# Optimization experiments

Hardware: AMD Instinct MI355X
Metric: run time of the kernel (lower is better)

## Reference

```python
import jax, jax.numpy as jnp
import numpy as np
import math

B, N, D = 4, 16384, 256
M, H = 64, 8
HD = D // H

def setup_inputs() -> dict:
    key = jax.random.key(0)
    ks = jax.random.split(key, 5)
    s = 1.0 / math.sqrt(D)
    return {
        "x": jax.random.normal(ks[0], (B, N, D), dtype=jnp.float32),
        "Ws": jax.random.normal(ks[1], (M, D), dtype=jnp.float32) * s,
        "bs": jnp.zeros((M,), dtype=jnp.float32),
        "Wqkv": jax.random.normal(ks[2], (3 * D, D), dtype=jnp.float32) * s,
        "Wo": jax.random.normal(ks[3], (D, D), dtype=jnp.float32) * s,
        "bo": jnp.zeros((D,), dtype=jnp.float32),
    }

def reference(x, Ws, bs, Wqkv, Wo, bo):
    # slice weights: softmax over N (dim=1), matching the torch code exactly
    logits = jnp.einsum('bnd,md->bnm', x, Ws) + bs          # [B,N,M]
    weights = jax.nn.softmax(logits, axis=1)                # softmax over N
    # pooling: tokens[b,m,d] = sum_n w[b,n,m] * x[b,n,d]
    tokens = jnp.einsum('bnm,bnd->bmd', weights, x)         # [B,M,D]
    # qkv projection (no bias)
    qkv = jnp.einsum('bmd,ed->bme', tokens, Wqkv)           # [B,M,3D]
    qkv = qkv.reshape(B, M, 3, H, HD)
    q = qkv[:, :, 0].transpose(0, 2, 1, 3)                  # [B,H,M,HD]
    k = qkv[:, :, 1].transpose(0, 2, 1, 3)
    v = qkv[:, :, 2].transpose(0, 2, 1, 3)
    scale = 1.0 / math.sqrt(HD)
    attn = jax.nn.softmax(jnp.einsum('bhmd,bhkd->bhmk', q, k) * scale, axis=-1)
    token_out = jnp.einsum('bhmk,bhkd->bhmd', attn, v)      # [B,H,M,HD]
    token_out = token_out.transpose(0, 2, 1, 3).reshape(B, M, D)
    token_out = jnp.einsum('bmd,ed->bme', token_out, Wo) + bo
    # unpooling: out[b,n,d] = sum_m w[b,n,m] * token_out[b,m,d]
    out = jnp.einsum('bnm,bmd->bnd', weights, token_out)    # [B,N,D]
    return out
```

## Files before the change

kernel.cpp:

```cpp
#include <hip/hip_runtime.h>
#include <math.h>

constexpr int B = 4;
constexpr int N = 16384;
constexpr int D = 256;
constexpr int M = 64;
constexpr int H = 8;

typedef __attribute__((ext_vector_type(8))) short short8;
typedef __attribute__((ext_vector_type(4))) float floatx4;

__device__ __forceinline__ float4 ld4(const float* p) {
  return *reinterpret_cast<const float4*>(p);
}
__device__ __forceinline__ unsigned short f2bf(float f) {
  unsigned u = __float_as_uint(f);
  unsigned r = (u + 0x7fffu + ((u >> 16) & 1u)) >> 16;
  return (unsigned short)r;
}

__global__ __launch_bounds__(256) void k0_prep(
    const float* __restrict__ Ws, const float* __restrict__ Wqkv,
    const float* __restrict__ Wo, unsigned short* __restrict__ WsB,
    unsigned short* __restrict__ WqkvB, unsigned short* __restrict__ WoB,
    float* __restrict__ denom, float* __restrict__ tokens) {
  const int g = blockIdx.x * 256 + threadIdx.x;
  if (g < 32768)
    *reinterpret_cast<float2*>(&tokens[g * 2]) = make_float2(0.f, 0.f);
  if (g < 128)
    *reinterpret_cast<float2*>(&denom[g * 2]) = make_float2(0.f, 0.f);
  const float* src;
  unsigned short* dst;
  int off;
  if (g < 2048) {
    src = Ws; dst = WsB; off = g;
  } else if (g < 26624) {
    src = Wqkv; dst = WqkvB; off = g - 2048;
  } else {
    src = Wo; dst = WoB; off = g - 26624;
  }
  const float4 a = ld4(&src[(size_t)off * 8]);
  const float4 c = ld4(&src[(size_t)off * 8 + 4]);
  unsigned d0 = (unsigned)f2bf(a.x) | ((unsigned)f2bf(a.y) << 16);
  unsigned d1 = (unsigned)f2bf(a.z) | ((unsigned)f2bf(a.w) << 16);
  unsigned d2 = (unsigned)f2bf(c.x) | ((unsigned)f2bf(c.y) << 16);
  unsigned d3 = (unsigned)f2bf(c.z) | ((unsigned)f2bf(c.w) << 16);
  *reinterpret_cast<uint4*>(&dst[(size_t)off * 8]) = make_uint4(d0, d1, d2, d3);
}

__global__ __launch_bounds__(512, 4) void k1_fused(
    const float* __restrict__ x, const unsigned short* __restrict__ WsB,
    const float* __restrict__ bs, unsigned short* __restrict__ En,
    float* __restrict__ denom) {
  __shared__ unsigned short Wt[64][264];
  __shared__ float red[64];
  const int b = blockIdx.y;
  const int n0 = blockIdx.x * 128;
  const int tid = threadIdx.x;
  const int w = tid >> 6, l = tid & 63;
  const int l15 = l & 15;
  const int q8 = (l >> 4) * 8;
  const int ar = w * 16 + l15;

  float4 fx[16];
  const float* xrow = &x[((size_t)(b * N + n0 + ar)) * D];
#pragma unroll
  for (int ks = 0; ks < 8; ++ks) {
    fx[2 * ks] = ld4(&xrow[ks * 32 + q8]);
    fx[2 * ks + 1] = ld4(&xrow[ks * 32 + q8 + 4]);
  }
#pragma unroll
  for (int p = 0; p < 4; ++p) {
    const int u = p * 512 + tid;
    const int row = u >> 5;
    const int c = (u & 31) * 8;
    *reinterpret_cast<short8*>(&Wt[row][c]) =
        *reinterpret_cast<const short8*>(&WsB[(size_t)row * 256 + c]);
  }
  if (tid < 64) red[tid] = 0.0f;

  short8 afr[8];
#pragma unroll
  for (int ks = 0; ks < 8; ++ks) {
    const float4 a0 = fx[2 * ks], a1 = fx[2 * ks + 1];
    short8 t;
    t[0] = (short)f2bf(a0.x); t[1] = (short)f2bf(a0.y);
    t[2] = (short)f2bf(a0.z); t[3] = (short)f2bf(a0.w);
    t[4] = (short)f2bf(a1.x); t[5] = (short)f2bf(a1.y);
    t[6] = (short)f2bf(a1.z); t[7] = (short)f2bf(a1.w);
    afr[ks] = t;
  }
  __syncthreads();

  floatx4 acc[4] = {{0.f, 0.f, 0.f, 0.f},
                    {0.f, 0.f, 0.f, 0.f},
                    {0.f, 0.f, 0.f, 0.f},
                    {0.f, 0.f, 0.f, 0.f}};
#pragma unroll
  for (int ks = 0; ks < 8; ++ks) {
#pragma unroll
    for (int mt = 0; mt < 4; ++mt) {
      short8 bf = *reinterpret_cast<short8*>(&Wt[mt * 16 + l15][ks * 32 + q8]);
      acc[mt] = __builtin_amdgcn_mfma_f32_16x16x32_bf16(afr[ks], bf, acc[mt], 0, 0, 0);
    }
  }

#pragma unroll
  for (int mt = 0; mt < 4; ++mt) {
    const int m = mt * 16 + l15;
    const float bsm = bs[m];
    float s = 0.0f;
#pragma unroll
    for (int r = 0; r < 4; ++r) {
      const int n = w * 16 + (l >> 4) * 4 + r;
      const float e = expf(acc[mt][r] + bsm);
      s += e;
      En[((size_t)(b * N + n0 + n)) * M + m] = f2bf(e);
    }
    atomicAdd(&red[m], s);
  }
  __syncthreads();
  if (tid < 64) atomicAdd(&denom[b * M + tid], red[tid]);
}

__global__ __launch_bounds__(256) void k2_pool(
    const unsigned short* __restrict__ En, const float* __restrict__ x,
    float* __restrict__ tokens) {
  __shared__ unsigned short Ens[64][70];
  __shared__ unsigned short XsT[64][72];
  const int dt = blockIdx.x, nc = blockIdx.y, b = blockIdx.z;
  const int d0 = dt * 64;
  const int tid = threadIdx.x;
  const int w = tid >> 6, l = tid & 63;
  const int l15 = l & 15;
  const int q8 = (l >> 4) * 8;
  floatx4 acc[4] = {{0.f, 0.f, 0.f, 0.f},
                    {0.f, 0.f, 0.f, 0.f},
                    {0.f, 0.f, 0.f, 0.f},
                    {0.f, 0.f, 0.f, 0.f}};
  for (int kc = 0; kc < 4; ++kc) {
    const int nb = nc * 256 + kc * 64;
    __syncthreads();
#pragma unroll
    for (int p = 0; p < 2; ++p) {
      const int u = p * 256 + tid;
      const int n = u >> 3;
      const int c8 = (u & 7) * 8;
      short8 v = *reinterpret_cast<const short8*>(
          &En[((size_t)(b * N + nb + n)) * M + c8]);
      uint4 uv = *reinterpret_cast<uint4*>(&v);
      unsigned* dp = reinterpret_cast<unsigned*>(&Ens[n][c8]);
      dp[0] = uv.x; dp[1] = uv.y; dp[2] = uv.z; dp[3] = uv.w;
    }
    {
      const int n = tid >> 2;
      const int c16 = (tid & 3) * 16;
      const float* xp = &x[((size_t)(b * N + nb + n)) * D + d0 + c16];
#pragma unroll
      for (int q = 0; q < 4; ++q) {
        float4 v = ld4(xp + q * 4);
        XsT[c16 + q * 4 + 0][n] = f2bf(v.x);
        XsT[c16 + q * 4 + 1][n] = f2bf(v.y);
        XsT[c16 + q * 4 + 2][n] = f2bf(v.z);
        XsT[c16 + q * 4 + 3][n] = f2bf(v.w);
      }
    }
    __syncthreads();
#pragma unroll
    for (int ks = 0; ks < 2; ++ks) {
      const int nf = ks * 32 + q8;
      short8 a;
#pragma unroll
      for (int j = 0; j < 8; ++j) a[j] = (short)Ens[nf + j][w * 16 + l15];
#pragma unroll
      for (int dtile = 0; dtile < 4; ++dtile) {
        short8 bf = *reinterpret_cast<short8*>(&XsT[dtile * 16 + l15][nf]);
        acc[dtile] =
            __builtin_amdgcn_mfma_f32_16x16x32_bf16(a, bf, acc[dtile], 0, 0, 0);
      }
    }
  }
#pragma unroll
  for (int dtile = 0; dtile < 4; ++dtile)
#pragma unroll
    for (int r = 0; r < 4; ++r) {
      const int m = w * 16 + (l >> 4) * 4 + r;
      const int d = d0 + dtile * 16 + (l & 15);
      atomicAdd(&tokens[((size_t)(b * M + m)) * D + d], acc[dtile][r]);
    }
}

__global__ __launch_bounds__(256) void k_proj(
    const float* __restrict__ A, const unsigned short* __restrict__ WB,
    const float* __restrict__ bias, const float* __restrict__ denom,
    float* __restrict__ OutF, unsigned short* __restrict__ OutT, const int EC,
    const int mode) {
  __shared__ unsigned short At[64][264];
  __shared__ unsigned short Wt[64][264];
  __shared__ float Cs[64][68];
  const int et = blockIdx.x;
  const int b = blockIdx.y;
  const int tid = threadIdx.x;
  const int w = tid >> 6, l = tid & 63;
#pragma unroll
  for (int p = 0; p < 16; ++p) {
    const int i = p * 256 + tid;
    const int row = i >> 6;
    const int c4 = (i & 63) * 4;
    float4 av = ld4(&A[((size_t)(b * M + row)) * D + c4]);
    unsigned a0 = (unsigned)f2bf(av.x) | ((unsigned)f2bf(av.y) << 16);
    unsigned a1 = (unsigned)f2bf(av.z) | ((unsigned)f2bf(av.w) << 16);
    *reinterpret_cast<uint2*>(&At[row][c4]) = make_uint2(a0, a1);
  }
#pragma unroll
  for (int p = 0; p < 8; ++p) {
    const int u = p * 256 + tid;
    const int row = u >> 5;
    const int c = (u & 31) * 8;
    *reinterpret_cast<short8*>(&Wt[row][c]) =
        *reinterpret_cast<const short8*>(&WB[((size_t)(et * 64 + row)) * 256 + c]);
  }
  __syncthreads();
  floatx4 acc[4] = {{0.f, 0.f, 0.f, 0.f},
                    {0.f, 0.f, 0.f, 0.f},
                    {0.f, 0.f, 0.f, 0.f},
                    {0.f, 0.f, 0.f, 0.f}};
  const int ar = w * 16 + (l & 15);
  const int q8 = (l >> 4) * 8;
#pragma unroll
  for (int ks = 0; ks < 8; ++ks) {
    short8 a = *reinterpret_cast<short8*>(&At[ar][ks * 32 + q8]);
#pragma unroll
    for (int mt = 0; mt < 4; ++mt) {
      short8 bf = *reinterpret_cast<short8*>(&Wt[mt * 16 + (l & 15)][ks * 32 + q8]);
      acc[mt] = __builtin_amdgcn_mfma_f32_16x16x32_bf16(a, bf, acc[mt], 0, 0, 0);
    }
  }
  if (mode == 0) {
#pragma unroll
    for (int mt = 0; mt < 4; ++mt) {
#pragma unroll
      for (int r = 0; r < 4; ++r) {
        const int row = w * 16 + (l >> 4) * 4 + r;
        const float rcp = 1.0f / denom[b * M + row];
        const int e = et * 64 + mt * 16 + (l & 15);
        OutF[((size_t)(b * M + row)) * EC + e] = acc[mt][r] * rcp;
      }
    }
  } else {
#pragma unroll
    for (int mt = 0; mt < 4; ++mt) {
#pragma unroll
      for (int r = 0; r < 4; ++r) {
        const int row = w * 16 + (l >> 4) * 4 + r;
        const float rcp = 1.0f / denom[b * M + row];
        const int el = mt * 16 + (l & 15);
        const float bv = bias[et * 64 + el];
        Cs[row][el] = (acc[mt][r] + bv) * rcp;
      }
    }
    __syncthreads();
#pragma unroll
    for (int p = 0; p < 2; ++p) {
      const int g = p * 256 + tid;
      const int e = g >> 3;
      const int m0 = (g & 7) * 8;
      unsigned short bu[8];
#pragma unroll
      for (int k = 0; k < 8; ++k) bu[k] = f2bf(Cs[m0 + k][e]);
      uint4 pk;
      pk.x = (unsigned)bu[0] | ((unsigned)bu[1] << 16);
      pk.y = (unsigned)bu[2] | ((unsigned)bu[3] << 16);
      pk.z = (unsigned)bu[4] | ((unsigned)bu[5] << 16);
      pk.w = (unsigned)bu[6] | ((unsigned)bu[7] << 16);
      *reinterpret_cast<uint4*>(
          &OutT[((size_t)(b * D + et * 64 + e)) * M + m0]) = pk;
    }
  }
}

__global__ __launch_bounds__(256) void k4_attn(
    const float* __restrict__ qkv, float* __restrict__ attn_o) {
  __shared__ float qt[32][68];
  __shared__ float kt[32][68];
  __shared__ float vv[64][36];
  __shared__ float P[64][68];
  const int b = blockIdx.x >> 3;
  const int h = blockIdx.x & 7;
  const int tid = threadIdx.x;
  for (int i = tid; i < 512; i += 256) {
    const int m = i >> 3;
    const int c4 = (i & 7) * 4;
    const float* base = &qkv[((size_t)(b * M + m)) * 768 + h * 32 + c4];
    float4 q4 = ld4(base);
    float4 k4 = ld4(base + 256);
    float4 v4 = ld4(base + 512);
    qt[c4 + 0][m] = q4.x; qt[c4 + 1][m] = q4.y; qt[c4 + 2][m] = q4.z; qt[c4 + 3][m] = q4.w;
    kt[c4 + 0][m] = k4.x; kt[c4 + 1][m] = k4.y; kt[c4 + 2][m] = k4.z; kt[c4 + 3][m] = k4.w;
    *reinterpret_cast<float4*>(&vv[m][c4]) = v4;
  }
  __syncthreads();
  {
    const int tm4 = (tid & 15) * 4;
    const int tn4 = (tid >> 4) * 4;
    float acc[4][4] = {};
    for (int k = 0; k < 32; ++k) {
      float4 a4 = ld4(&qt[k][tn4]);
      float4 b4 = ld4(&kt[k][tm4]);
#pragma unroll
      for (int i = 0; i < 4; ++i) {
        const float av = (i == 0) ? a4.x : (i == 1) ? a4.y : (i == 2) ? a4.z : a4.w;
        acc[i][0] = fmaf(av, b4.x, acc[i][0]);
        acc[i][1] = fmaf(av, b4.y, acc[i][1]);
        acc[i][2] = fmaf(av, b4.z, acc[i][2]);
        acc[i][3] = fmaf(av, b4.w, acc[i][3]);
      }
    }
    const float scale = 0.17677669529663687f;
#pragma unroll
    for (int i = 0; i < 4; ++i)
      *reinterpret_cast<float4*>(&P[tn4 + i][tm4]) =
          make_float4(acc[i][0] * scale, acc[i][1] * scale, acc[i][2] * scale,
                      acc[i][3] * scale);
  }
  __syncthreads();
  if (tid < 64) {
    float mx = -1e30f;
    for (int j = 0; j < 64; ++j) mx = fmaxf(mx, P[tid][j]);
    float s = 0.0f;
    for (int j = 0; j < 64; ++j) {
      const float e = expf(P[tid][j] - mx);
      P[tid][j] = e;
      s += e;
    }
    const float r = 1.0f / s;
    for (int j = 0; j < 64; ++j) P[tid][j] *= r;
  }
  __syncthreads();
  if (tid < 128) {
    const int i0 = (tid >> 3) * 4;
    const int c0 = (tid & 7) * 4;
    float o[4][4] = {};
    for (int j = 0; j < 64; ++j) {
      float4 v4 = ld4(&vv[j][c0]);
#pragma unroll
      for (int ii = 0; ii < 4; ++ii) {
        const float p = P[i0 + ii][j];
        o[ii][0] = fmaf(p, v4.x, o[ii][0]);
        o[ii][1] = fmaf(p, v4.y, o[ii][1]);
        o[ii][2] = fmaf(p, v4.z, o[ii][2]);
        o[ii][3] = fmaf(p, v4.w, o[ii][3]);
      }
    }
#pragma unroll
    for (int ii = 0; ii < 4; ++ii)
      *reinterpret_cast<float4*>(
          &attn_o[((size_t)(b * M + i0 + ii)) * D + h * 32 + c0]) =
          make_float4(o[ii][0], o[ii][1], o[ii][2], o[ii][3]);
  }
}

__global__ __launch_bounds__(256) void k6_unpool(
    const unsigned short* __restrict__ En, const unsigned short* __restrict__ TpT,
    float* __restrict__ out) {
  __shared__ unsigned short EnS[64][72];
  __shared__ unsigned short TpS[64][72];
  const int dt = blockIdx.x, nt = blockIdx.y, b = blockIdx.z;
  const int n0 = nt * 64, d0 = dt * 64;
  const int tid = threadIdx.x;
  const int w = tid >> 6, l = tid & 63;
#pragma unroll
  for (int p = 0; p < 2; ++p) {
    const int g = p * 256 + tid;
    const int row = g >> 3;
    const int c8 = (g & 7) * 8;
    *reinterpret_cast<short8*>(&EnS[row][c8]) =
        *reinterpret_cast<const short8*>(
            &En[((size_t)(b * N + n0 + row)) * M + c8]);
    *reinterpret_cast<short8*>(&TpS[row][c8]) =
        *reinterpret_cast<const short8*>(
            &TpT[((size_t)(b * D + d0 + row)) * M + c8]);
  }
  __syncthreads();
  floatx4 acc[4] = {{0.f, 0.f, 0.f, 0.f},
                    {0.f, 0.f, 0.f, 0.f},
                    {0.f, 0.f, 0.f, 0.f},
                    {0.f, 0.f, 0.f, 0.f}};
  const int q8 = (l >> 4) * 8;
#pragma unroll
  for (int ks = 0; ks < 2; ++ks) {
    short8 a = *reinterpret_cast<short8*>(&EnS[w * 16 + (l & 15)][ks * 32 + q8]);
#pragma unroll
    for (int dtile = 0; dtile < 4; ++dtile) {
      short8 bf = *reinterpret_cast<short8*>(
          &TpS[dtile * 16 + (l & 15)][ks * 32 + q8]);
      acc[dtile] =
          __builtin_amdgcn_mfma_f32_16x16x32_bf16(a, bf, acc[dtile], 0, 0, 0);
    }
  }
#pragma unroll
  for (int dtile = 0; dtile < 4; ++dtile)
#pragma unroll
    for (int r = 0; r < 4; ++r) {
      const int n = n0 + w * 16 + (l >> 4) * 4 + r;
      const int d = d0 + dtile * 16 + (l & 15);
      out[((size_t)(b * N + n)) * D + d] = acc[dtile][r];
    }
}

extern "C" void kernel_launch(void* const* d_in, const int* in_sizes, int n_in,
                              void* d_out, int out_size, void* d_ws,
                              size_t ws_size, hipStream_t stream) {
  const float* x = (const float*)d_in[0];
  const float* Ws = (const float*)d_in[1];
  const float* bs = (const float*)d_in[2];
  const float* Wqkv = (const float*)d_in[3];
  const float* Wo = (const float*)d_in[4];
  const float* bo = (const float*)d_in[5];
  float* out = (float*)d_out;

  char* p = (char*)d_ws;
  unsigned short* En = (unsigned short*)p;    p += (size_t)B * N * M * 2;
  unsigned short* TpT = (unsigned short*)p;   p += (size_t)B * D * M * 2;
  float* denom = (float*)p;                   p += (size_t)B * M * 4;
  float* tokens = (float*)p;                  p += (size_t)B * M * D * 4;
  float* qkv = (float*)p;                     p += (size_t)B * M * 3 * D * 4;
  float* attn_o = (float*)p;                  p += (size_t)B * M * D * 4;
  unsigned short* WsB = (unsigned short*)p;   p += (size_t)M * D * 2;
  unsigned short* WqkvB = (unsigned short*)p; p += (size_t)3 * D * D * 2;
  unsigned short* WoB = (unsigned short*)p;   p += (size_t)D * D * 2;

  k0_prep<<<dim3(136), 256, 0, stream>>>(Ws, Wqkv, Wo, WsB, WqkvB, WoB,
                                         denom, tokens);
  k1_fused<<<dim3(N / 128, B), 512, 0, stream>>>(x, WsB, bs, En, denom);
  k2_pool<<<dim3(D / 64, N / 256, B), 256, 0, stream>>>(En, x, tokens);
  k_proj<<<dim3(12, B), 256, 0, stream>>>(tokens, WqkvB, nullptr, denom, qkv,
                                          nullptr, 768, 0);
  k4_attn<<<dim3(B * H), 256, 0, stream>>>(qkv, attn_o);
  k_proj<<<dim3(4, B), 256, 0, stream>>>(attn_o, WoB, bo, denom, nullptr, TpT,
                                         256, 1);
  k6_unpool<<<dim3(D / 64, N / 64, B), 256, 0, stream>>>(En, TpT, out);
}
```

Measured before the change: 180.1 us.

## Fuse QKV projection, attention and output projection into one per-head kernel

Result: faster. 174.6 us (-3.0%).

```diff
diff --git a/kernel.cpp b/kernel.cpp
--- a/kernel.cpp
+++ b/kernel.cpp
@@ -23,10 +23,13 @@
     const float* __restrict__ Ws, const float* __restrict__ Wqkv,
     const float* __restrict__ Wo, unsigned short* __restrict__ WsB,
     unsigned short* __restrict__ WqkvB, unsigned short* __restrict__ WoB,
-    float* __restrict__ denom, float* __restrict__ tokens) {
+    float* __restrict__ denom, float* __restrict__ tokens,
+    float* __restrict__ tokO) {
   const int g = blockIdx.x * 256 + threadIdx.x;
-  if (g < 32768)
+  if (g < 32768) {
     *reinterpret_cast<float2*>(&tokens[g * 2]) = make_float2(0.f, 0.f);
+    *reinterpret_cast<float2*>(&tokO[g * 2]) = make_float2(0.f, 0.f);
+  }
   if (g < 128)
     *reinterpret_cast<float2*>(&denom[g * 2]) = make_float2(0.f, 0.f);
   const float* src;
@@ -190,151 +193,123 @@
     }
 }
 
-__global__ __launch_bounds__(256) void k_proj(
-    const float* __restrict__ A, const unsigned short* __restrict__ WB,
-    const float* __restrict__ bias, const float* __restrict__ denom,
-    float* __restrict__ OutF, unsigned short* __restrict__ OutT, const int EC,
-    const int mode) {
-  __shared__ unsigned short At[64][264];
-  __shared__ unsigned short Wt[64][264];
-  __shared__ float Cs[64][68];
-  const int et = blockIdx.x;
-  const int b = blockIdx.y;
+__global__ __launch_bounds__(256) void k_fa(
+    const float* __restrict__ tokens, const unsigned short* __restrict__ WqkvB,
+    const unsigned short* __restrict__ WoB, const float* __restrict__ denom,
+    float* __restrict__ tokO) {
+  __shared__ __align__(16) char smem[84480];
+  unsigned short* const At = reinterpret_cast<unsigned short*>(smem);
+  unsigned short* const Wq = reinterpret_cast<unsigned short*>(smem + 33792);
+  float* const qt = reinterpret_cast<float*>(smem);
+  float* const kt = reinterpret_cast<float*>(smem + 8704);
+  float* const vv = reinterpret_cast<float*>(smem + 17408);
+  float* const P  = reinterpret_cast<float*>(smem + 26624);
+  float* const ao = reinterpret_cast<float*>(smem + 44032);
+  const int b = blockIdx.x >> 3;
+  const int h = blockIdx.x & 7;
   const int tid = threadIdx.x;
   const int w = tid >> 6, l = tid & 63;
+  const int l15 = l & 15;
+  const int q8 = (l >> 4) * 8;
+  const int r4 = (l >> 4) * 4;
+
 #pragma unroll
   for (int p = 0; p < 16; ++p) {
     const int i = p * 256 + tid;
     const int row = i >> 6;
     const int c4 = (i & 63) * 4;
-    float4 av = ld4(&A[((size_t)(b * M + row)) * D + c4]);
+    float4 av = ld4(&tokens[((size_t)(b * M + row)) * D + c4]);
     unsigned a0 = (unsigned)f2bf(av.x) | ((unsigned)f2bf(av.y) << 16);
     unsigned a1 = (unsigned)f2bf(av.z) | ((unsigned)f2bf(av.w) << 16);
-    *reinterpret_cast<uint2*>(&At[row][c4]) = make_uint2(a0, a1);
-  }
-#pragma unroll
-  for (int p = 0; p < 8; ++p) {
+    *reinterpret_cast<uint2*>(&At[row * 264 + c4]) = make_uint2(a0, a1);
+  }
+#pragma unroll
+  for (int p = 0; p < 12; ++p) {
     const int u = p * 256 + tid;
     const int row = u >> 5;
     const int c = (u & 31) * 8;
-    *reinterpret_cast<short8*>(&Wt[row][c]) =
-        *reinterpret_cast<const short8*>(&WB[((size_t)(et * 64 + row)) * 256 + c]);
-  }
-  __syncthreads();
-  floatx4 acc[4] = {{0.f, 0.f, 0.f, 0.f},
-                    {0.f, 0.f, 0.f, 0.f},
-                    {0.f, 0.f, 0.f, 0.f},
-                    {0.f, 0.f, 0.f, 0.f}};
-  const int ar = w * 16 + (l & 15);
-  const int q8 = (l >> 4) * 8;
+    const int eg = (row < 32) ? (h * 32 + row)
+                 : (row < 64) ? (256 + h * 32 + row - 32)
+                              : (512 + h * 32 + row - 64);
+    *reinterpret_cast<short8*>(&Wq[row * 264 + c]) =
+        *reinterpret_cast<const short8*>(&WqkvB[(size_t)eg * 256 + c]);
+  }
+  float rcp4[4];
+#pragma unroll
+  for (int r = 0; r < 4; ++r)
+    rcp4[r] = 1.0f / denom[b * M + w * 16 + r4 + r];
+  __syncthreads();
+
+  floatx4 acc[6] = {{0.f, 0.f, 0.f, 0.f}, {0.f, 0.f, 0.f, 0.f},
+                    {0.f, 0.f, 0.f, 0.f}, {0.f, 0.f, 0.f, 0.f},
+                    {0.f, 0.f, 0.f, 0.f}, {0.f, 0.f, 0.f, 0.f}};
+  const int arow = w * 16 + l15;
 #pragma unroll
   for (int ks = 0; ks < 8; ++ks) {
-    short8 a = *reinterpret_cast<short8*>(&At[ar][ks * 32 + q8]);
-#pragma unroll
-    for (int mt = 0; mt < 4; ++mt) {
-      short8 bf = *reinterpret_cast<short8*>(&Wt[mt * 16 + (l & 15)][ks * 32 + q8]);
-      acc[mt] = __builtin_amdgcn_mfma_f32_16x16x32_bf16(a, bf, acc[mt], 0, 0, 0);
-    }
-  }
-  if (mode == 0) {
-#pragma unroll
-    for (int mt = 0; mt < 4; ++mt) {
-#pragma unroll
-      for (int r = 0; r < 4; ++r) {
-        const int row = w * 16 + (l >> 4) * 4 + r;
-        const float rcp = 1.0f / denom[b * M + row];
-        const int e = et * 64 + mt * 16 + (l & 15);
-        OutF[((size_t)(b * M + row)) * EC + e] = acc[mt][r] * rcp;
-      }
-    }
-  } else {
-#pragma unroll
-    for (int mt = 0; mt < 4; ++mt) {
-#pragma unroll
-      for (int r = 0; r < 4; ++r) {
-        const int row = w * 16 + (l >> 4) * 4 + r;
-        const float rcp = 1.0f / denom[b * M + row];
-        const int el = mt * 16 + (l & 15);
-        const float bv = bias[et * 64 + el];
-        Cs[row][el] = (acc[mt][r] + bv) * rcp;
-      }
-    }
-    __syncthreads();
-#pragma unroll
-    for (int p = 0; p < 2; ++p) {
-      const int g = p * 256 + tid;
-      const int e = g >> 3;
-      const int m0 = (g & 7) * 8;
-      unsigned short bu[8];
-#pragma unroll
-      for (int k = 0; k < 8; ++k) bu[k] = f2bf(Cs[m0 + k][e]);
-      uint4 pk;
-      pk.x = (unsigned)bu[0] | ((unsigned)bu[1] << 16);
-      pk.y = (unsigned)bu[2] | ((unsigned)bu[3] << 16);
-      pk.z = (unsigned)bu[4] | ((unsigned)bu[5] << 16);
-      pk.w = (unsigned)bu[6] | ((unsigned)bu[7] << 16);
-      *reinterpret_cast<uint4*>(
-          &OutT[((size_t)(b * D + et * 64 + e)) * M + m0]) = pk;
-    }
-  }
-}
-
-__global__ __launch_bounds__(256) void k4_attn(
-    const float* __restrict__ qkv, float* __restrict__ attn_o) {
-  __shared__ float qt[32][68];
-  __shared__ float kt[32][68];
-  __shared__ float vv[64][36];
-  __shared__ float P[64][68];
-  const int b = blockIdx.x >> 3;
-  const int h = blockIdx.x & 7;
-  const int tid = threadIdx.x;
-  for (int i = tid; i < 512; i += 256) {
-    const int m = i >> 3;
-    const int c4 = (i & 7) * 4;
-    const float* base = &qkv[((size_t)(b * M + m)) * 768 + h * 32 + c4];
-    float4 q4 = ld4(base);
-    float4 k4 = ld4(base + 256);
-    float4 v4 = ld4(base + 512);
-    qt[c4 + 0][m] = q4.x; qt[c4 + 1][m] = q4.y; qt[c4 + 2][m] = q4.z; qt[c4 + 3][m] = q4.w;
-    kt[c4 + 0][m] = k4.x; kt[c4 + 1][m] = k4.y; kt[c4 + 2][m] = k4.z; kt[c4 + 3][m] = k4.w;
-    *reinterpret_cast<float4*>(&vv[m][c4]) = v4;
-  }
-  __syncthreads();
+    short8 a = *reinterpret_cast<short8*>(&At[arow * 264 + ks * 32 + q8]);
+#pragma unroll
+    for (int et = 0; et < 6; ++et) {
+      short8 bf = *reinterpret_cast<short8*>(&Wq[(et * 16 + l15) * 264 + ks * 32 + q8]);
+      acc[et] = __builtin_amdgcn_mfma_f32_16x16x32_bf16(a, bf, acc[et], 0, 0, 0);
+    }
+  }
+  short8 wof[4];
+#pragma unroll
+  for (int dt4 = 0; dt4 < 4; ++dt4)
+    wof[dt4] = *reinterpret_cast<const short8*>(
+        &WoB[(size_t)(w * 64 + dt4 * 16 + l15) * 256 + h * 32 + q8]);
+  __syncthreads();
+
+#pragma unroll
+  for (int r = 0; r < 4; ++r) {
+    const int m = w * 16 + r4 + r;
+    const float rc = rcp4[r];
+#pragma unroll
+    for (int et = 0; et < 6; ++et) {
+      const float val = acc[et][r] * rc;
+      const int c = (et & 1) * 16 + l15;
+      if (et < 2) qt[c * 68 + m] = val;
+      else if (et < 4) kt[c * 68 + m] = val;
+      else vv[m * 36 + c] = val;
+    }
+  }
+  __syncthreads();
+
   {
     const int tm4 = (tid & 15) * 4;
     const int tn4 = (tid >> 4) * 4;
-    float acc[4][4] = {};
+    float sacc[4][4] = {};
     for (int k = 0; k < 32; ++k) {
-      float4 a4 = ld4(&qt[k][tn4]);
-      float4 b4 = ld4(&kt[k][tm4]);
+      float4 a4 = ld4(&qt[k * 68 + tn4]);
+      float4 b4 = ld4(&kt[k * 68 + tm4]);
 #pragma unroll
       for (int i = 0; i < 4; ++i) {
         const float av = (i == 0) ? a4.x : (i == 1) ? a4.y : (i == 2) ? a4.z : a4.w;
-        acc[i][0] = fmaf(av, b4.x, acc[i][0]);
-        acc[i][1] = fmaf(av, b4.y, acc[i][1]);
-        acc[i][2] = fmaf(av, b4.z, acc[i][2]);
-        acc[i][3] = fmaf(av, b4.w, acc[i][3]);
+        sacc[i][0] = fmaf(av, b4.x, sacc[i][0]);
+        sacc[i][1] = fmaf(av, b4.y, sacc[i][1]);
+        sacc[i][2] = fmaf(av, b4.z, sacc[i][2]);
+        sacc[i][3] = fmaf(av, b4.w, sacc[i][3]);
       }
     }
     const float scale = 0.17677669529663687f;
 #pragma unroll
     for (int i = 0; i < 4; ++i)
-      *reinterpret_cast<float4*>(&P[tn4 + i][tm4]) =
-          make_float4(acc[i][0] * scale, acc[i][1] * scale, acc[i][2] * scale,
-                      acc[i][3] * scale);
+      *reinterpret_cast<float4*>(&P[(tn4 + i) * 68 + tm4]) =
+          make_float4(sacc[i][0] * scale, sacc[i][1] * scale,
+                      sacc[i][2] * scale, sacc[i][3] * scale);
   }
   __syncthreads();
   if (tid < 64) {
     float mx = -1e30f;
-    for (int j = 0; j < 64; ++j) mx = fmaxf(mx, P[tid][j]);
+    for (int j = 0; j < 64; ++j) mx = fmaxf(mx, P[tid * 68 + j]);
     float s = 0.0f;
     for (int j = 0; j < 64; ++j) {
-      const float e = expf(P[tid][j] - mx);
-      P[tid][j] = e;
+      const float e = expf(P[tid * 68 + j] - mx);
+      P[tid * 68 + j] = e;
       s += e;
     }
     const float r = 1.0f / s;
-    for (int j = 0; j < 64; ++j) P[tid][j] *= r;
+    for (int j = 0; j < 64; ++j) P[tid * 68 + j] *= r;
   }
   __syncthreads();
   if (tid < 128) {
@@ -342,10 +317,10 @@
     const int c0 = (tid & 7) * 4;
     float o[4][4] = {};
     for (int j = 0; j < 64; ++j) {
-      float4 v4 = ld4(&vv[j][c0]);
+      float4 v4 = ld4(&vv[j * 36 + c0]);
 #pragma unroll
       for (int ii = 0; ii < 4; ++ii) {
-        const float p = P[i0 + ii][j];
+        const float p = P[(i0 + ii) * 68 + j];
         o[ii][0] = fmaf(p, v4.x, o[ii][0]);
         o[ii][1] = fmaf(p, v4.y, o[ii][1]);
         o[ii][2] = fmaf(p, v4.z, o[ii][2]);
@@ -354,46 +329,94 @@
     }
 #pragma unroll
     for (int ii = 0; ii < 4; ++ii)
-      *reinterpret_cast<float4*>(
-          &attn_o[((size_t)(b * M + i0 + ii)) * D + h * 32 + c0]) =
-          make_float4(o[ii][0], o[ii][1], o[ii][2], o[ii][3]);
-  }
-}
-
-__global__ __launch_bounds__(256) void k6_unpool(
-    const unsigned short* __restrict__ En, const unsigned short* __restrict__ TpT,
+#pragma unroll
+      for (int jj = 0; jj < 4; ++jj) ao[(i0 + ii) * 36 + c0 + jj] = o[ii][jj];
+  }
+  __syncthreads();
+
+  floatx4 acc2[4][4] = {{{0.f, 0.f, 0.f, 0.f}, {0.f, 0.f, 0.f, 0.f},
+                         {0.f, 0.f, 0.f, 0.f}, {0.f, 0.f, 0.f, 0.f}},
+                        {{0.f, 0.f, 0.f, 0.f}, {0.f, 0.f, 0.f, 0.f},
+                         {0.f, 0.f, 0.f, 0.f}, {0.f, 0.f, 0.f, 0.f}},
+                        {{0.f, 0.f, 0.f, 0.f}, {0.f, 0.f, 0.f, 0.f},
+                         {0.f, 0.f, 0.f, 0.f}, {0.f, 0.f, 0.f, 0.f}},
+                        {{0.f, 0.f, 0.f, 0.f}, {0.f, 0.f, 0.f, 0.f},
+                         {0.f, 0.f, 0.f, 0.f}, {0.f, 0.f, 0.f, 0.f}}};
+#pragma unroll
+  for (int mt = 0; mt < 4; ++mt) {
+    short8 af;
+#pragma unroll
+    for (int j = 0; j < 8; ++j)
+      af[j] = (short)f2bf(ao[(mt * 16 + l15) * 36 + q8 + j]);
+#pragma unroll
+    for (int dt4 = 0; dt4 < 4; ++dt4)
+      acc2[mt][dt4] =
+          __builtin_amdgcn_mfma_f32_16x16x32_bf16(af, wof[dt4], acc2[mt][dt4], 0, 0, 0);
+  }
+#pragma unroll
+  for (int mt = 0; mt < 4; ++mt)
+#pragma unroll
+    for (int dt4 = 0; dt4 < 4; ++dt4)
+#pragma unroll
+      for (int r = 0; r < 4; ++r) {
+        const int m = mt * 16 + r4 + r;
+        const int d = w * 64 + dt4 * 16 + l15;
+        atomicAdd(&tokO[((size_t)(b * M + m)) * D + d], acc2[mt][dt4][r]);
+      }
+}
+
+__global__ __launch_bounds__(512, 4) void k6_unpool(
+    const unsigned short* __restrict__ En, const float* __restrict__ tokO,
+    const float* __restrict__ denom, const float* __restrict__ bo,
     float* __restrict__ out) {
-  __shared__ unsigned short EnS[64][72];
+  __shared__ unsigned short EnS[128][72];
   __shared__ unsigned short TpS[64][72];
   const int dt = blockIdx.x, nt = blockIdx.y, b = blockIdx.z;
-  const int n0 = nt * 64, d0 = dt * 64;
+  const int n0 = nt * 128, d0 = dt * 64;
   const int tid = threadIdx.x;
   const int w = tid >> 6, l = tid & 63;
+  const int l15 = l & 15;
+  const int q8 = (l >> 4) * 8;
 #pragma unroll
   for (int p = 0; p < 2; ++p) {
-    const int g = p * 256 + tid;
+    const int g = p * 512 + tid;
     const int row = g >> 3;
     const int c8 = (g & 7) * 8;
     *reinterpret_cast<short8*>(&EnS[row][c8]) =
         *reinterpret_cast<const short8*>(
             &En[((size_t)(b * N + n0 + row)) * M + c8]);
-    *reinterpret_cast<short8*>(&TpS[row][c8]) =
-        *reinterpret_cast<const short8*>(
-            &TpT[((size_t)(b * D + d0 + row)) * M + c8]);
+  }
+  {
+    const int m = tid >> 3;
+    const int c8 = (tid & 7) * 8;
+    const float rc = 1.0f / denom[b * M + m];
+    const float* tp = &tokO[((size_t)(b * M + m)) * D + d0 + c8];
+    float4 v0 = ld4(tp);
+    float4 v1 = ld4(tp + 4);
+    float4 bb0 = ld4(&bo[d0 + c8]);
+    float4 bb1 = ld4(&bo[d0 + c8 + 4]);
+    TpS[c8 + 0][m] = f2bf((v0.x + bb0.x) * rc);
+    TpS[c8 + 1][m] = f2bf((v0.y + bb0.y) * rc);
+    TpS[c8 + 2][m] = f2bf((v0.z + bb0.z) * rc);
+    TpS[c8 + 3][m] = f2bf((v0.w + bb0.w) * rc);
+    TpS[c8 + 4][m] = f2bf((v1.x + bb1.x) * rc);
+    TpS[c8 + 5][m] = f2bf((v1.y + bb1.y) * rc);
+    TpS[c8 + 6][m] = f2bf((v1.z + bb1.z) * rc);
+    TpS[c8 + 7][m] = f2bf((v1.w + bb1.w) * rc);
   }
   __syncthreads();
   floatx4 acc[4] = {{0.f, 0.f, 0.f, 0.f},
                     {0.f, 0.f, 0.f, 0.f},
                     {0.f, 0.f, 0.f, 0.f},
                     {0.f, 0.f, 0.f, 0.f}};
-  const int q8 = (l >> 4) * 8;
+  const int arow = w * 16 + l15;
 #pragma unroll
   for (int ks = 0; ks < 2; ++ks) {
-    short8 a = *reinterpret_cast<short8*>(&EnS[w * 16 + (l & 15)][ks * 32 + q8]);
+    short8 a = *reinterpret_cast<short8*>(&EnS[arow][ks * 32 + q8]);
 #pragma unroll
     for (int dtile = 0; dtile < 4; ++dtile) {
       short8 bf = *reinterpret_cast<short8*>(
-          &TpS[dtile * 16 + (l & 15)][ks * 32 + q8]);
+          &TpS[dtile * 16 + l15][ks * 32 + q8]);
       acc[dtile] =
           __builtin_amdgcn_mfma_f32_16x16x32_bf16(a, bf, acc[dtile], 0, 0, 0);
     }
@@ -403,7 +426,7 @@
 #pragma unroll
     for (int r = 0; r < 4; ++r) {
       const int n = n0 + w * 16 + (l >> 4) * 4 + r;
-      const int d = d0 + dtile * 16 + (l & 15);
+      const int d = d0 + dtile * 16 + l15;
       out[((size_t)(b * N + n)) * D + d] = acc[dtile][r];
     }
 }
@@ -421,23 +444,18 @@
 
   char* p = (char*)d_ws;
   unsigned short* En = (unsigned short*)p;    p += (size_t)B * N * M * 2;
-  unsigned short* TpT = (unsigned short*)p;   p += (size_t)B * D * M * 2;
   float* denom = (float*)p;                   p += (size_t)B * M * 4;
   float* tokens = (float*)p;                  p += (size_t)B * M * D * 4;
-  float* qkv = (float*)p;                     p += (size_t)B * M * 3 * D * 4;
-  float* attn_o = (float*)p;                  p += (size_t)B * M * D * 4;
+  float* tokO = (float*)p;                    p += (size_t)B * M * D * 4;
   unsigned short* WsB = (unsigned short*)p;   p += (size_t)M * D * 2;
   unsigned short* WqkvB = (unsigned short*)p; p += (size_t)3 * D * D * 2;
   unsigned short* WoB = (unsigned short*)p;   p += (size_t)D * D * 2;
 
   k0_prep<<<dim3(136), 256, 0, stream>>>(Ws, Wqkv, Wo, WsB, WqkvB, WoB,
-                                         denom, tokens);
+                                         denom, tokens, tokO);
   k1_fused<<<dim3(N / 128, B), 512, 0, stream>>>(x, WsB, bs, En, denom);
   k2_pool<<<dim3(D / 64, N / 256, B), 256, 0, stream>>>(En, x, tokens);
-  k_proj<<<dim3(12, B), 256, 0, stream>>>(tokens, WqkvB, nullptr, denom, qkv,
-                                          nullptr, 768, 0);
-  k4_attn<<<dim3(B * H), 256, 0, stream>>>(qkv, attn_o);
-  k_proj<<<dim3(4, B), 256, 0, stream>>>(attn_o, WoB, bo, denom, nullptr, TpT,
-                                         256, 1);
-  k6_unpool<<<dim3(D / 64, N / 64, B), 256, 0, stream>>>(En, TpT, out);
-}
+  k_fa<<<dim3(B * H), 256, 0, stream>>>(tokens, WqkvB, WoB, denom, tokO);
+  k6_unpool<<<dim3(D / 64, N / 128, B), 512, 0, stream>>>(En, tokO, denom, bo,
+                                                          out);
+}
```
